# Performance work log

Hardware: AMD Instinct MI355X
Metric: run time of the kernel (lower is better)

Reference implementation:

```python
import jax, jax.numpy as jnp
import numpy as np

N = 16384
E = 262144
HID = 128
NFILT = 128
NGAUSS = 50
NINTER = 6
CUTOFF = 10.0
NUMZ = 100
LOG2 = 0.6931471805599453


def ssp(x):
    # ShiftedSoftplus
    return jax.nn.softplus(x) - LOG2


def setup_inputs() -> dict:
    key = jax.random.key(0)
    ks = jax.random.split(key, 20)
    z = jax.random.randint(ks[0], (N,), 0, NUMZ)
    pos = jax.random.uniform(ks[1], (N, 3), dtype=jnp.float32) * 5.0  # box side 5 -> all pairs < cutoff
    edge_index = jax.random.randint(ks[2], (2, E), 0, N)
    s = lambda k, shape, fan: jax.random.normal(k, shape, dtype=jnp.float32) / np.sqrt(fan)
    params = dict(
        emb=s(ks[3], (NUMZ, HID), 1.0),
        Wf1=s(ks[4], (NINTER, NGAUSS, NFILT), NGAUSS), bf1=jnp.zeros((NINTER, NFILT), jnp.float32),
        Wf2=s(ks[5], (NINTER, NFILT, NFILT), NFILT), bf2=jnp.zeros((NINTER, NFILT), jnp.float32),
        Wl1=s(ks[6], (NINTER, HID, NFILT), HID),
        Wl2=s(ks[7], (NINTER, NFILT, HID), NFILT), bl2=jnp.zeros((NINTER, HID), jnp.float32),
        Wl=s(ks[8], (NINTER, HID, HID), HID), bl=jnp.zeros((NINTER, HID), jnp.float32),
        Wo1=s(ks[9], (HID, HID // 2), HID), bo1=jnp.zeros((HID // 2,), jnp.float32),
        Wo2=s(ks[10], (HID // 2, 1), HID // 2), bo2=jnp.zeros((1,), jnp.float32),
    )
    return dict(z=z, pos=pos, edge_index=edge_index, **params)


def reference(z, pos, edge_index, emb, Wf1, bf1, Wf2, bf2, Wl1, Wl2, bl2, Wl, bl, Wo1, bo1, Wo2, bo2):
    src, dst = edge_index[0], edge_index[1]
    # edge distances and Gaussian smearing
    d = jnp.linalg.norm(pos[src] - pos[dst], axis=-1)          # [E]
    offset = jnp.linspace(0.0, CUTOFF, NGAUSS, dtype=jnp.float32)
    coeff = -0.5 / (offset[1] - offset[0]) ** 2
    ea = jnp.exp(coeff * (d[:, None] - offset) ** 2)            # [E, NGAUSS]
    C = 0.5 * (jnp.cos(d * (np.pi / CUTOFF)) + 1.0)             # cosine cutoff [E]

    h = emb[z]                                                  # [N, HID]
    for i in range(NINTER):
        # continuous-filter weights
        Wfilt = (ssp(ea @ Wf1[i] + bf1[i]) @ Wf2[i] + bf2[i]) * C[:, None]  # [E, NFILT]
        x = h @ Wl1[i]                                          # lin1, no bias [N, NFILT]
        msg = x[src] * Wfilt                                    # gather + filter
        agg = jax.ops.segment_sum(msg, dst, num_segments=N)     # scatter-sum [N, NFILT]
        x = ssp(agg @ Wl2[i] + bl2[i]) @ Wl[i] + bl[i]          # lin2 -> ssp -> lin
        h = h + x

    h = ssp(h @ Wo1 + bo1) @ Wo2 + bo2                          # [N, 1] per-atom energy
    out = jnp.sum(h, axis=0, keepdims=True)                     # 'add' readout, single graph -> [1, 1]
    return jax.nn.relu(out)
```

## Files before the change

### kernel.cpp

```cpp
#include <hip/hip_runtime.h>
#include <math.h>

#define NATOM 16384
#define NEDGE 262144
#define HID 128
#define NG 50
#define NI 6

typedef _Float16 h8_t __attribute__((ext_vector_type(8)));
typedef _Float16 h4_t __attribute__((ext_vector_type(4)));
typedef float    f4_t __attribute__((ext_vector_type(4)));

__device__ __forceinline__ float ssp_f(float v) {
    float e = __expf(-fabsf(v));
    return fmaxf(v, 0.0f) + __logf(1.0f + e) - 0.69314718055994531f;
}

__global__ void fill0(float* __restrict__ p, int n4) {
    int i = blockIdx.x * 256 + threadIdx.x;
    if (i < n4) ((float4*)p)[i] = make_float4(0.f, 0.f, 0.f, 0.f);
}

__global__ void hist_k(const int* __restrict__ ei, int* __restrict__ cnt) {
    int e = blockIdx.x * 256 + threadIdx.x;
    if (e < NEDGE) atomicAdd(&cnt[ei[NEDGE + e]], 1);
}

__global__ void scan_k(const int* __restrict__ cnt, int* __restrict__ offs) {
    __shared__ int part[256];
    int t = threadIdx.x;
    int base = t * 64;
    int s = 0;
    for (int i = 0; i < 64; ++i) s += cnt[base + i];
    part[t] = s;
    __syncthreads();
    for (int off = 1; off < 256; off <<= 1) {
        int v = (t >= off) ? part[t - off] : 0;
        __syncthreads();
        part[t] += v;
        __syncthreads();
    }
    int r = part[t] - s;
    for (int i = 0; i < 64; ++i) { offs[base + i] = r; r += cnt[base + i]; }
    if (t == 255) offs[NATOM] = r;
}

__global__ void scatter_k(const int* __restrict__ ei, const int* __restrict__ offs,
                          int* __restrict__ cnt, int* __restrict__ sSrc, int* __restrict__ sDst) {
    int e = blockIdx.x * 256 + threadIdx.x;
    if (e >= NEDGE) return;
    int d = ei[NEDGE + e];
    int r = atomicAdd(&cnt[d], 1);
    int j = offs[d] + r;
    sSrc[j] = ei[e];
    sDst[j] = d;
}

__global__ void edge_pre(const float* __restrict__ pos,
                         const int* __restrict__ sSrc, const int* __restrict__ sDst,
                         _Float16* __restrict__ ea, float* __restrict__ Cb) {
    int j = blockIdx.x * 256 + threadIdx.x;
    if (j >= NEDGE) return;
    int s = sSrc[j], dd = sDst[j];
    float dx = pos[3*s]   - pos[3*dd];
    float dy = pos[3*s+1] - pos[3*dd+1];
    float dz = pos[3*s+2] - pos[3*dd+2];
    float d = sqrtf(dx*dx + dy*dy + dz*dz);
    Cb[j] = 0.5f * (cosf(d * 0.31415926535897931f) + 1.0f);
    const float delta = 10.0f / 49.0f;
    const float coeff = -0.5f / (delta * delta);
    #pragma unroll
    for (int gq = 0; gq < 8; ++gq) {
        h8_t hv;
        #pragma unroll
        for (int r = 0; r < 8; ++r) {
            int g = gq * 8 + r;
            float v = 0.0f;
            if (g < NG) { float u = d - (float)g * delta; v = __expf(coeff * u * u); }
            hv[r] = (_Float16)v;
        }
        *(h8_t*)&ea[(size_t)j * 64 + gq * 8] = hv;
    }
}

__global__ void wprep(const float* __restrict__ Wf1, const float* __restrict__ Wf2,
                      const float* __restrict__ Wl1, const float* __restrict__ Wl2,
                      const float* __restrict__ Wl,
                      _Float16* __restrict__ w1, _Float16* __restrict__ w2,
                      _Float16* __restrict__ wnh, _Float16* __restrict__ wnl) {
    int idx = blockIdx.x * 256 + threadIdx.x;
    const int S1 = NI * 128 * 64, S2 = NI * 128 * 128;
    if (idx < S1) {
        int i = idx >> 13, r = idx & 8191, fo = r >> 6, k = r & 63;
        float v = (k < NG) ? Wf1[(size_t)i * NG * 128 + k * 128 + fo] : 0.0f;
        w1[idx] = (_Float16)v;
        return;
    }
    idx -= S1;
    if (idx < S2) {
        int i = idx >> 14, r = idx & 16383, fo = r >> 7, k = r & 127;
        w2[idx] = (_Float16)Wf2[(size_t)i * 128 * 128 + k * 128 + fo];
        return;
    }
    idx -= S2;
    if (idx < 3 * S2) {
        int mi = idx >> 14;
        int r = idx & 16383, fo = r >> 7, k = r & 127;
        int m = mi / NI, i = mi % NI;
        const float* W = (m == 0) ? Wl1 : (m == 1) ? Wl2 : Wl;
        float v = W[(size_t)i * 128 * 128 + k * 128 + fo];
        _Float16 hh = (_Float16)v;
        wnh[idx] = hh; wnl[idx] = (_Float16)(v - (float)hh);
    }
}

__global__ void embed_k(const int* __restrict__ z, const float* __restrict__ emb,
                        float* __restrict__ h) {
    int tid = blockIdx.x * 256 + threadIdx.x;
    int n = tid >> 7, f = tid & 127;
    h[tid] = emb[z[n] * HID + f];
}

__launch_bounds__(256)
__global__ void gemm_node_mfma(const float* __restrict__ A,
                               const _Float16* __restrict__ wth, const _Float16* __restrict__ wtl,
                               _Float16* __restrict__ xh) {
    __shared__ _Float16 aH[64 * 136];
    __shared__ _Float16 aL[64 * 136];
    int t = threadIdx.x;
    int mb = blockIdx.x * 64;
    #pragma unroll
    for (int j = 0; j < 8; ++j) {
        int idx = t + j * 256;
        int row = idx >> 5, c4 = idx & 31;
        f4_t v = *(const f4_t*)&A[(size_t)(mb + row) * HID + c4 * 4];
        h4_t hh, ll;
        #pragma unroll
        for (int r = 0; r < 4; ++r) {
            _Float16 hx = (_Float16)v[r];
            hh[r] = hx; ll[r] = (_Float16)(v[r] - (float)hx);
        }
        *(h4_t*)&aH[row * 136 + c4 * 4] = hh;
        *(h4_t*)&aL[row * 136 + c4 * 4] = ll;
    }
    __syncthreads();

    int wv = t >> 6, lane = t & 63, l15 = lane & 15, quad = lane >> 4;
    f4_t acc[2][4];
    #pragma unroll
    for (int m = 0; m < 2; ++m)
        #pragma unroll
        for (int n = 0; n < 4; ++n) acc[m][n] = (f4_t)0.0f;

    for (int kc = 0; kc < 4; ++kc) {
        int k0 = kc * 32 + quad * 8;
        h8_t a_h[2], a_l[2];
        #pragma unroll
        for (int m = 0; m < 2; ++m) {
            int fr = wv * 32 + m * 16 + l15;
            a_h[m] = *(const h8_t*)&wth[fr * 128 + k0];
            a_l[m] = *(const h8_t*)&wtl[fr * 128 + k0];
        }
        #pragma unroll
        for (int n = 0; n < 4; ++n) {
            int er = n * 16 + l15;
            h8_t b_h = *(const h8_t*)&aH[er * 136 + k0];
            h8_t b_l = *(const h8_t*)&aL[er * 136 + k0];
            #pragma unroll
            for (int m = 0; m < 2; ++m) {
                acc[m][n] = __builtin_amdgcn_mfma_f32_16x16x32_f16(a_h[m], b_h, acc[m][n], 0, 0, 0);
                acc[m][n] = __builtin_amdgcn_mfma_f32_16x16x32_f16(a_h[m], b_l, acc[m][n], 0, 0, 0);
                acc[m][n] = __builtin_amdgcn_mfma_f32_16x16x32_f16(a_l[m], b_h, acc[m][n], 0, 0, 0);
            }
        }
    }

    #pragma unroll
    for (int n = 0; n < 4; ++n) {
        int el = n * 16 + l15;
        size_t row = (size_t)(mb + el);
        #pragma unroll
        for (int m = 0; m < 2; ++m) {
            int fb = wv * 32 + m * 16 + quad * 4;
            h4_t o;
            #pragma unroll
            for (int r = 0; r < 4; ++r) o[r] = (_Float16)acc[m][n][r];
            *(h4_t*)&xh[row * 128 + fb] = o;
        }
    }
}

__launch_bounds__(256)
__global__ void gemm_node3(const float* __restrict__ agg,
                           const _Float16* __restrict__ w2th, const _Float16* __restrict__ w2tl,
                           const _Float16* __restrict__ wlth, const _Float16* __restrict__ wltl,
                           const _Float16* __restrict__ w1nh, const _Float16* __restrict__ w1nl,
                           const float* __restrict__ bl2, const float* __restrict__ bl,
                           float* __restrict__ h, _Float16* __restrict__ xh) {
    __shared__ _Float16 aH[64 * 136];
    __shared__ _Float16 aL[64 * 136];
    int t = threadIdx.x;
    int mb = blockIdx.x * 64;
    #pragma unroll
    for (int j = 0; j < 8; ++j) {
        int idx = t + j * 256;
        int row = idx >> 5, c4 = idx & 31;
        f4_t v = *(const f4_t*)&agg[(size_t)(mb + row) * HID + c4 * 4];
        h4_t hh, ll;
        #pragma unroll
        for (int r = 0; r < 4; ++r) {
            _Float16 hx = (_Float16)v[r];
            hh[r] = hx; ll[r] = (_Float16)(v[r] - (float)hx);
        }
        *(h4_t*)&aH[row * 136 + c4 * 4] = hh;
        *(h4_t*)&aL[row * 136 + c4 * 4] = ll;
    }
    __syncthreads();

    int wv = t >> 6, lane = t & 63, l15 = lane & 15, quad = lane >> 4;
    int fq = wv * 32 + quad * 4;
    f4_t acc[2][4];

    #pragma unroll
    for (int m = 0; m < 2; ++m)
        #pragma unroll
        for (int n = 0; n < 4; ++n) acc[m][n] = (f4_t)0.0f;
    for (int kc = 0; kc < 4; ++kc) {
        int k0 = kc * 32 + quad * 8;
        h8_t a_h[2], a_l[2];
        #pragma unroll
        for (int m = 0; m < 2; ++m) {
            int fr = wv * 32 + m * 16 + l15;
            a_h[m] = *(const h8_t*)&w2th[fr * 128 + k0];
            a_l[m] = *(const h8_t*)&w2tl[fr * 128 + k0];
        }
        #pragma unroll
        for (int n = 0; n < 4; ++n) {
            int er = n * 16 + l15;
            h8_t b_h = *(const h8_t*)&aH[er * 136 + k0];
            h8_t b_l = *(const h8_t*)&aL[er * 136 + k0];
            #pragma unroll
            for (int m = 0; m < 2; ++m) {
                acc[m][n] = __builtin_amdgcn_mfma_f32_16x16x32_f16(a_h[m], b_h, acc[m][n], 0, 0, 0);
                acc[m][n] = __builtin_amdgcn_mfma_f32_16x16x32_f16(a_h[m], b_l, acc[m][n], 0, 0, 0);
                acc[m][n] = __builtin_amdgcn_mfma_f32_16x16x32_f16(a_l[m], b_h, acc[m][n], 0, 0, 0);
            }
        }
    }
    f4_t b2v[2];
    b2v[0] = *(const f4_t*)&bl2[fq]; b2v[1] = *(const f4_t*)&bl2[fq + 16];
    __syncthreads();

    #pragma unroll
    for (int m = 0; m < 2; ++m)
        #pragma unroll
        for (int n = 0; n < 4; ++n) {
            int el = n * 16 + l15;
            int fb = wv * 32 + m * 16 + quad * 4;
            h4_t hh, ll;
            #pragma unroll
            for (int r = 0; r < 4; ++r) {
                float sv = ssp_f(acc[m][n][r] + b2v[m][r]);
                _Float16 hx = (_Float16)sv;
                hh[r] = hx;
                ll[r] = (_Float16)(sv - (float)hx);
            }
            *(h4_t*)&aH[el * 136 + fb] = hh;
            *(h4_t*)&aL[el * 136 + fb] = ll;
        }
    __syncthreads();

    #pragma unroll
    for (int m = 0; m < 2; ++m)
        #pragma unroll
        for (int n = 0; n < 4; ++n) acc[m][n] = (f4_t)0.0f;
    for (int kc = 0; kc < 4; ++kc) {
        int k0 = kc * 32 + quad * 8;
        h8_t a_h[2], a_l[2];
        #pragma unroll
        for (int m = 0; m < 2; ++m) {
            int fr = wv * 32 + m * 16 + l15;
            a_h[m] = *(const h8_t*)&wlth[fr * 128 + k0];
            a_l[m] = *(const h8_t*)&wltl[fr * 128 + k0];
        }
        #pragma unroll
        for (int n = 0; n < 4; ++n) {
            int er = n * 16 + l15;
            h8_t b_h = *(const h8_t*)&aH[er * 136 + k0];
            h8_t b_l = *(const h8_t*)&aL[er * 136 + k0];
            #pragma unroll
            for (int m = 0; m < 2; ++m) {
                acc[m][n] = __builtin_amdgcn_mfma_f32_16x16x32_f16(a_h[m], b_h, acc[m][n], 0, 0, 0);
                acc[m][n] = __builtin_amdgcn_mfma_f32_16x16x32_f16(a_h[m], b_l, acc[m][n], 0, 0, 0);
                acc[m][n] = __builtin_amdgcn_mfma_f32_16x16x32_f16(a_l[m], b_h, acc[m][n], 0, 0, 0);
            }
        }
    }
    f4_t blv[2];
    blv[0] = *(const f4_t*)&bl[fq]; blv[1] = *(const f4_t*)&bl[fq + 16];
    __syncthreads();

    #pragma unroll
    for (int n = 0; n < 4; ++n) {
        int el = n * 16 + l15;
        size_t row = (size_t)(mb + el);
        #pragma unroll
        for (int m = 0; m < 2; ++m) {
            int fb = wv * 32 + m * 16 + quad * 4;
            f4_t hv = *(const f4_t*)&h[row * 128 + fb];
            f4_t o;
            h4_t hh, ll;
            #pragma unroll
            for (int r = 0; r < 4; ++r) {
                o[r] = hv[r] + acc[m][n][r] + blv[m][r];
                _Float16 hx = (_Float16)o[r];
                hh[r] = hx; ll[r] = (_Float16)(o[r] - (float)hx);
            }
            *(f4_t*)&h[row * 128 + fb] = o;
            *(h4_t*)&aH[el * 136 + fb] = hh;
            *(h4_t*)&aL[el * 136 + fb] = ll;
        }
    }
    if (!w1nh) return;
    __syncthreads();

    #pragma unroll
    for (int m = 0; m < 2; ++m)
        #pragma unroll
        for (int n = 0; n < 4; ++n) acc[m][n] = (f4_t)0.0f;
    for (int kc = 0; kc < 4; ++kc) {
        int k0 = kc * 32 + quad * 8;
        h8_t a_h[2], a_l[2];
        #pragma unroll
        for (int m = 0; m < 2; ++m) {
            int fr = wv * 32 + m * 16 + l15;
            a_h[m] = *(const h8_t*)&w1nh[fr * 128 + k0];
            a_l[m] = *(const h8_t*)&w1nl[fr * 128 + k0];
        }
        #pragma unroll
        for (int n = 0; n < 4; ++n) {
            int er = n * 16 + l15;
            h8_t b_h = *(const h8_t*)&aH[er * 136 + k0];
            h8_t b_l = *(const h8_t*)&aL[er * 136 + k0];
            #pragma unroll
            for (int m = 0; m < 2; ++m) {
                acc[m][n] = __builtin_amdgcn_mfma_f32_16x16x32_f16(a_h[m], b_h, acc[m][n], 0, 0, 0);
                acc[m][n] = __builtin_amdgcn_mfma_f32_16x16x32_f16(a_h[m], b_l, acc[m][n], 0, 0, 0);
                acc[m][n] = __builtin_amdgcn_mfma_f32_16x16x32_f16(a_l[m], b_h, acc[m][n], 0, 0, 0);
            }
        }
    }
    #pragma unroll
    for (int n = 0; n < 4; ++n) {
        int el = n * 16 + l15;
        size_t row = (size_t)(mb + el);
        #pragma unroll
        for (int m = 0; m < 2; ++m) {
            int fb = wv * 32 + m * 16 + quad * 4;
            h4_t o;
            #pragma unroll
            for (int r = 0; r < 4; ++r) o[r] = (_Float16)acc[m][n][r];
            *(h4_t*)&xh[row * 128 + fb] = o;
        }
    }
}

#define T1_LDW 136
#define EA_LDW 72
#define NDST 16

__launch_bounds__(256, 4)
__global__ void edge_filter(const _Float16* __restrict__ xh, float* __restrict__ agg,
                            const int* __restrict__ sSrc, const int* __restrict__ sDst,
                            const int* __restrict__ offs, const float* __restrict__ Cb,
                            const _Float16* __restrict__ ea,
                            const _Float16* __restrict__ w1, const _Float16* __restrict__ w2,
                            const float* __restrict__ bf1, const float* __restrict__ bf2) {
    __shared__ __align__(16) _Float16 eaS[64 * EA_LDW];
    __shared__ __align__(16) _Float16 t1S[64 * T1_LDW];
    __shared__ float accS[NDST * 128];
    __shared__ int dstl[64];

    _Float16* msg = t1S;

    int t = threadIdx.x;
    int wv = t >> 6, lane = t & 63;
    int l15 = lane & 15, quad = lane >> 4;
    int d0 = blockIdx.x * NDST;
    int estart = offs[d0];
    int ecnt = offs[d0 + NDST] - estart;
    int tmax = (ecnt + 63) >> 6;

    #pragma unroll
    for (int c = 0; c < 2; ++c)
        *(f4_t*)&accS[(t + c * 256) * 4] = (f4_t)0.0f;

    h8_t w1f[2][2], w2f[4][2];
    #pragma unroll
    for (int kc = 0; kc < 2; ++kc) {
        int k0 = kc * 32 + quad * 8;
        #pragma unroll
        for (int m = 0; m < 2; ++m)
            w1f[kc][m] = *(const h8_t*)&w1[(wv * 32 + m * 16 + l15) * 64 + k0];
    }
    #pragma unroll
    for (int kc = 0; kc < 4; ++kc) {
        int k0 = kc * 32 + quad * 8;
        #pragma unroll
        for (int m = 0; m < 2; ++m)
            w2f[kc][m] = *(const h8_t*)&w2[(wv * 32 + m * 16 + l15) * 128 + k0];
    }
    int fq = wv * 32 + quad * 4;
    f4_t b1v[2], b2v[2];
    b1v[0] = *(const f4_t*)&bf1[fq];  b1v[1] = *(const f4_t*)&bf1[fq + 16];
    b2v[0] = *(const f4_t*)&bf2[fq];  b2v[1] = *(const f4_t*)&bf2[fq + 16];

    for (int tt = 0; tt < tmax; ++tt) {
        int base = estart + tt * 64;
        int lim = ecnt - tt * 64;

        #pragma unroll
        for (int c = 0; c < 2; ++c) {
            int ch = t + c * 256;
            int e = ch >> 3, ks = ch & 7;
            h8_t v = (h8_t)(_Float16)0.0f;
            if (e < lim) v = *(const h8_t*)&ea[(size_t)(base + e) * 64 + ks * 8];
            *(h8_t*)&eaS[e * EA_LDW + ks * 8] = v;
        }
        if (t < 64) {
            int dl = 0;
            if (t < lim) dl = sDst[base + t] - d0;
            dstl[t] = dl;
        }
        int srcn[4];
        float cn[4];
        #pragma unroll
        for (int n = 0; n < 4; ++n) {
            int rel = n * 16 + l15;
            bool ok = rel < lim;
            srcn[n] = ok ? sSrc[base + rel] : 0;
            cn[n]   = ok ? Cb[base + rel] : 0.0f;
        }
        h4_t xr[4][2];
        #pragma unroll
        for (int n = 0; n < 4; ++n)
            #pragma unroll
            for (int m = 0; m < 2; ++m)
                xr[n][m] = *(const h4_t*)&xh[(size_t)srcn[n] * HID + wv * 32 + m * 16 + quad * 4];
        __syncthreads();

        f4_t acc1[2][4];
        #pragma unroll
        for (int m = 0; m < 2; ++m)
            #pragma unroll
            for (int n = 0; n < 4; ++n) acc1[m][n] = (f4_t)0.0f;
        #pragma unroll
        for (int kc = 0; kc < 2; ++kc) {
            int k0 = kc * 32 + quad * 8;
            h8_t b[4];
            #pragma unroll
            for (int n = 0; n < 4; ++n)
                b[n] = *(const h8_t*)&eaS[(n * 16 + l15) * EA_LDW + k0];
            #pragma unroll
            for (int m = 0; m < 2; ++m)
                #pragma unroll
                for (int n = 0; n < 4; ++n)
                    acc1[m][n] = __builtin_amdgcn_mfma_f32_16x16x32_f16(w1f[kc][m], b[n], acc1[m][n], 0, 0, 0);
        }

        #pragma unroll
        for (int m = 0; m < 2; ++m)
            #pragma unroll
            for (int n = 0; n < 4; ++n) {
                int el = n * 16 + l15;
                int fb = wv * 32 + m * 16 + quad * 4;
                h4_t hh;
                #pragma unroll
                for (int r = 0; r < 4; ++r)
                    hh[r] = (_Float16)ssp_f(acc1[m][n][r] + b1v[m][r]);
                *(h4_t*)&t1S[el * T1_LDW + fb] = hh;
            }
        __syncthreads();

        f4_t acc2[2][4];
        #pragma unroll
        for (int m = 0; m < 2; ++m)
            #pragma unroll
            for (int n = 0; n < 4; ++n) acc2[m][n] = (f4_t)0.0f;
        #pragma unroll
        for (int kc = 0; kc < 4; ++kc) {
            int k0 = kc * 32 + quad * 8;
            #pragma unroll
            for (int n = 0; n < 4; ++n) {
                h8_t b = *(const h8_t*)&t1S[(n * 16 + l15) * T1_LDW + k0];
                #pragma unroll
                for (int m = 0; m < 2; ++m)
                    acc2[m][n] = __builtin_amdgcn_mfma_f32_16x16x32_f16(w2f[kc][m], b, acc2[m][n], 0, 0, 0);
            }
        }
        __syncthreads();

        #pragma unroll
        for (int n = 0; n < 4; ++n) {
            int el = n * 16 + l15;
            float ce = cn[n];
            #pragma unroll
            for (int m = 0; m < 2; ++m) {
                int fb = wv * 32 + m * 16 + quad * 4;
                h4_t o;
                #pragma unroll
                for (int r = 0; r < 4; ++r)
                    o[r] = (_Float16)((acc2[m][n][r] + b2v[m][r]) * ce * (float)xr[n][m][r]);
                *(h4_t*)&msg[el * T1_LDW + fb] = o;
            }
        }
        __syncthreads();

        {
            int f = t & 127, hf = t >> 7;
            int ib = hf * 32;
            float run = 0.0f;
            int cur = dstl[ib];
            for (int i = ib; i < ib + 32; ++i) {
                int dnow = dstl[i];
                if (dnow != cur) {
                    atomicAdd(&accS[cur * 128 + f], run);
                    run = 0.0f;
                    cur = dnow;
                }
                run += (float)msg[i * T1_LDW + f];
            }
            atomicAdd(&accS[cur * 128 + f], run);
        }
        __syncthreads();
    }

    float* dstp = &agg[(size_t)d0 * HID];
    #pragma unroll
    for (int c = 0; c < 2; ++c) {
        int idx = t + c * 256;
        *(f4_t*)&dstp[idx * 4] = *(const f4_t*)&accS[idx * 4];
    }
}

__launch_bounds__(256)
__global__ void readout1(const float* __restrict__ h, const float* __restrict__ Wo1,
                         const float* __restrict__ bo1, const float* __restrict__ Wo2,
                         const float* __restrict__ bo2, float* __restrict__ accum) {
    __shared__ float w1[128 * 64];
    __shared__ float part[4];
    int t = threadIdx.x;
    for (int i = t; i < 128 * 16; i += 256)
        ((float4*)w1)[i] = ((const float4*)Wo1)[i];
    __syncthreads();
    int f = t & 63, wv = t >> 6;
    float b = bo1[f], w2v = Wo2[f];
    float lsum = 0.0f;
    for (int a = 0; a < 16; ++a) {
        int n = blockIdx.x * 64 + wv * 16 + a;
        const float* hr = &h[(size_t)n * HID];
        float acc = b;
        #pragma unroll 16
        for (int k = 0; k < 128; ++k)
            acc = fmaf(hr[k], w1[k*64 + f], acc);
        lsum += ssp_f(acc) * w2v;
    }
    #pragma unroll
    for (int off = 32; off > 0; off >>= 1)
        lsum += __shfl_down(lsum, off, 64);
    if (f == 0) part[wv] = lsum;
    __syncthreads();
    if (t == 0)
        atomicAdd(accum, part[0] + part[1] + part[2] + part[3] + 64.0f * bo2[0]);
}

__global__ void readout2(const float* __restrict__ accum, float* __restrict__ out) {
    out[0] = fmaxf(accum[0], 0.0f);
}

extern "C" void kernel_launch(void* const* d_in, const int* in_sizes, int n_in,
                              void* d_out, int out_size, void* d_ws, size_t ws_size,
                              hipStream_t stream) {
    const int*   z   = (const int*)d_in[0];
    const float* pos = (const float*)d_in[1];
    const int*   ei  = (const int*)d_in[2];
    const float* emb = (const float*)d_in[3];
    const float* Wf1 = (const float*)d_in[4];
    const float* bf1 = (const float*)d_in[5];
    const float* Wf2 = (const float*)d_in[6];
    const float* bf2 = (const float*)d_in[7];
    const float* Wl1 = (const float*)d_in[8];
    const float* Wl2 = (const float*)d_in[9];
    const float* bl2 = (const float*)d_in[10];
    const float* Wl  = (const float*)d_in[11];
    const float* bl  = (const float*)d_in[12];
    const float* Wo1 = (const float*)d_in[13];
    const float* bo1 = (const float*)d_in[14];
    const float* Wo2 = (const float*)d_in[15];
    const float* bo2 = (const float*)d_in[16];
    float* out = (float*)d_out;

    _Float16* w1  = (_Float16*)d_ws;
    _Float16* w2  = w1 + NI * 8192;
    _Float16* wnh = w2 + NI * 16384;
    _Float16* wnl = wnh + 3 * NI * 16384;
    _Float16* ea  = wnl + 3 * NI * 16384;
    _Float16* xh  = ea + (size_t)NEDGE * 64;
    float* Cb  = (float*)(xh + (size_t)NATOM * 128);
    float* h   = Cb + NEDGE;
    float* agg = h + (size_t)NATOM * HID;
    float* accum = agg + (size_t)NATOM * HID;
    int* cnt  = (int*)(accum + 4);
    int* offs = cnt + NATOM;
    int* sSrc = offs + NATOM + 4;
    int* sDst = sSrc + NEDGE;

    fill0<<<NATOM/4/256, 256, 0, stream>>>((float*)cnt, NATOM/4);
    hist_k<<<NEDGE/256, 256, 0, stream>>>(ei, cnt);
    scan_k<<<1, 256, 0, stream>>>(cnt, offs);
    fill0<<<NATOM/4/256, 256, 0, stream>>>((float*)cnt, NATOM/4);
    scatter_k<<<NEDGE/256, 256, 0, stream>>>(ei, offs, cnt, sSrc, sDst);

    edge_pre<<<NEDGE/256, 256, 0, stream>>>(pos, sSrc, sDst, ea, Cb);
    wprep<<<(NI*8192 + NI*16384 + 3*NI*16384)/256, 256, 0, stream>>>(
        Wf1, Wf2, Wl1, Wl2, Wl, w1, w2, wnh, wnl);
    embed_k<<<(NATOM*HID)/256, 256, 0, stream>>>(z, emb, h);

    gemm_node_mfma<<<256, 256, 0, stream>>>(h, wnh + (size_t)0*16384,
        wnl + (size_t)0*16384, xh);
    for (int i = 0; i < NI; ++i) {
        edge_filter<<<NATOM/NDST, 256, 0, stream>>>(xh, agg, sSrc, sDst, offs, Cb, ea,
            w1 + (size_t)i*8192, w2 + (size_t)i*16384,
            bf1 + i*HID, bf2 + i*HID);
        const _Float16* w1nh = (i < NI-1) ? wnh + (size_t)(i+1)*16384 : nullptr;
        const _Float16* w1nl = (i < NI-1) ? wnl + (size_t)(i+1)*16384 : nullptr;
        gemm_node3<<<256, 256, 0, stream>>>(agg,
            wnh + (size_t)(1*NI+i)*16384, wnl + (size_t)(1*NI+i)*16384,
            wnh + (size_t)(2*NI+i)*16384, wnl + (size_t)(2*NI+i)*16384,
            w1nh, w1nl, bl2 + i*HID, bl + i*HID, h, xh);
    }
    fill0<<<1, 256, 0, stream>>>(accum, 1);
    readout1<<<NATOM/64, 256, 0, stream>>>(h, Wo1, bo1, Wo2, bo2, accum);
    readout2<<<1, 1, 0, stream>>>(accum, out);
}
```

Before: 784.3 us.

## Drop split-fp16 node GEMMs, halve tiles, prefetch edge tiles in filter kernel

After: 1.093 ms. 1.39x slower.

```diff
diff --git a/kernel.cpp b/kernel.cpp
--- a/kernel.cpp
+++ b/kernel.cpp
@@ -87,7 +87,7 @@
                       const float* __restrict__ Wl1, const float* __restrict__ Wl2,
                       const float* __restrict__ Wl,
                       _Float16* __restrict__ w1, _Float16* __restrict__ w2,
-                      _Float16* __restrict__ wnh, _Float16* __restrict__ wnl) {
+                      _Float16* __restrict__ wn) {
     int idx = blockIdx.x * 256 + threadIdx.x;
     const int S1 = NI * 128 * 64, S2 = NI * 128 * 128;
     if (idx < S1) {
@@ -108,9 +108,7 @@
         int r = idx & 16383, fo = r >> 7, k = r & 127;
         int m = mi / NI, i = mi % NI;
         const float* W = (m == 0) ? Wl1 : (m == 1) ? Wl2 : Wl;
-        float v = W[(size_t)i * 128 * 128 + k * 128 + fo];
-        _Float16 hh = (_Float16)v;
-        wnh[idx] = hh; wnl[idx] = (_Float16)(v - (float)hh);
+        wn[idx] = (_Float16)W[(size_t)i * 128 * 128 + k * 128 + fo];
     }
 }
 
@@ -123,10 +121,9 @@
 
 __launch_bounds__(256)
 __global__ void gemm_node_mfma(const float* __restrict__ A,
-                               const _Float16* __restrict__ wth, const _Float16* __restrict__ wtl,
+                               const _Float16* __restrict__ wt,
                                _Float16* __restrict__ xh) {
-    __shared__ _Float16 aH[64 * 136];
-    __shared__ _Float16 aL[64 * 136];
+    __shared__ _Float16 aS[64 * 136];
     int t = threadIdx.x;
     int mb = blockIdx.x * 64;
     #pragma unroll
@@ -134,14 +131,10 @@
         int idx = t + j * 256;
         int row = idx >> 5, c4 = idx & 31;
         f4_t v = *(const f4_t*)&A[(size_t)(mb + row) * HID + c4 * 4];
-        h4_t hh, ll;
-        #pragma unroll
-        for (int r = 0; r < 4; ++r) {
-            _Float16 hx = (_Float16)v[r];
-            hh[r] = hx; ll[r] = (_Float16)(v[r] - (float)hx);
-        }
-        *(h4_t*)&aH[row * 136 + c4 * 4] = hh;
-        *(h4_t*)&aL[row * 136 + c4 * 4] = ll;
+        h4_t hh;
+        #pragma unroll
+        for (int r = 0; r < 4; ++r) hh[r] = (_Float16)v[r];
+        *(h4_t*)&aS[row * 136 + c4 * 4] = hh;
     }
     __syncthreads();
 
@@ -154,24 +147,16 @@
 
     for (int kc = 0; kc < 4; ++kc) {
         int k0 = kc * 32 + quad * 8;
-        h8_t a_h[2], a_l[2];
-        #pragma unroll
-        for (int m = 0; m < 2; ++m) {
-            int fr = wv * 32 + m * 16 + l15;
-            a_h[m] = *(const h8_t*)&wth[fr * 128 + k0];
-            a_l[m] = *(const h8_t*)&wtl[fr * 128 + k0];
-        }
+        h8_t a[2];
+        #pragma unroll
+        for (int m = 0; m < 2; ++m)
+            a[m] = *(const h8_t*)&wt[(wv * 32 + m * 16 + l15) * 128 + k0];
         #pragma unroll
         for (int n = 0; n < 4; ++n) {
-            int er = n * 16 + l15;
-            h8_t b_h = *(const h8_t*)&aH[er * 136 + k0];
-            h8_t b_l = *(const h8_t*)&aL[er * 136 + k0];
-            #pragma unroll
-            for (int m = 0; m < 2; ++m) {
-                acc[m][n] = __builtin_amdgcn_mfma_f32_16x16x32_f16(a_h[m], b_h, acc[m][n], 0, 0, 0);
-                acc[m][n] = __builtin_amdgcn_mfma_f32_16x16x32_f16(a_h[m], b_l, acc[m][n], 0, 0, 0);
-                acc[m][n] = __builtin_amdgcn_mfma_f32_16x16x32_f16(a_l[m], b_h, acc[m][n], 0, 0, 0);
-            }
+            h8_t b = *(const h8_t*)&aS[(n * 16 + l15) * 136 + k0];
+            #pragma unroll
+            for (int m = 0; m < 2; ++m)
+                acc[m][n] = __builtin_amdgcn_mfma_f32_16x16x32_f16(a[m], b, acc[m][n], 0, 0, 0);
         }
     }
 
@@ -192,59 +177,45 @@
 
 __launch_bounds__(256)
 __global__ void gemm_node3(const float* __restrict__ agg,
-                           const _Float16* __restrict__ w2th, const _Float16* __restrict__ w2tl,
-                           const _Float16* __restrict__ wlth, const _Float16* __restrict__ wltl,
-                           const _Float16* __restrict__ w1nh, const _Float16* __restrict__ w1nl,
+                           const _Float16* __restrict__ w2t, const _Float16* __restrict__ wlt,
+                           const _Float16* __restrict__ w1n,
                            const float* __restrict__ bl2, const float* __restrict__ bl,
                            float* __restrict__ h, _Float16* __restrict__ xh) {
-    __shared__ _Float16 aH[64 * 136];
-    __shared__ _Float16 aL[64 * 136];
+    __shared__ _Float16 aS[32 * 136];
     int t = threadIdx.x;
-    int mb = blockIdx.x * 64;
-    #pragma unroll
-    for (int j = 0; j < 8; ++j) {
+    int mb = blockIdx.x * 32;
+    #pragma unroll
+    for (int j = 0; j < 4; ++j) {
         int idx = t + j * 256;
         int row = idx >> 5, c4 = idx & 31;
         f4_t v = *(const f4_t*)&agg[(size_t)(mb + row) * HID + c4 * 4];
-        h4_t hh, ll;
-        #pragma unroll
-        for (int r = 0; r < 4; ++r) {
-            _Float16 hx = (_Float16)v[r];
-            hh[r] = hx; ll[r] = (_Float16)(v[r] - (float)hx);
-        }
-        *(h4_t*)&aH[row * 136 + c4 * 4] = hh;
-        *(h4_t*)&aL[row * 136 + c4 * 4] = ll;
+        h4_t hh;
+        #pragma unroll
+        for (int r = 0; r < 4; ++r) hh[r] = (_Float16)v[r];
+        *(h4_t*)&aS[row * 136 + c4 * 4] = hh;
     }
     __syncthreads();
 
     int wv = t >> 6, lane = t & 63, l15 = lane & 15, quad = lane >> 4;
     int fq = wv * 32 + quad * 4;
-    f4_t acc[2][4];
+    f4_t acc[2][2];
 
     #pragma unroll
     for (int m = 0; m < 2; ++m)
         #pragma unroll
-        for (int n = 0; n < 4; ++n) acc[m][n] = (f4_t)0.0f;
+        for (int n = 0; n < 2; ++n) acc[m][n] = (f4_t)0.0f;
     for (int kc = 0; kc < 4; ++kc) {
         int k0 = kc * 32 + quad * 8;
-        h8_t a_h[2], a_l[2];
-        #pragma unroll
-        for (int m = 0; m < 2; ++m) {
-            int fr = wv * 32 + m * 16 + l15;
-            a_h[m] = *(const h8_t*)&w2th[fr * 128 + k0];
-            a_l[m] = *(const h8_t*)&w2tl[fr * 128 + k0];
-        }
-        #pragma unroll
-        for (int n = 0; n < 4; ++n) {
-            int er = n * 16 + l15;
-            h8_t b_h = *(const h8_t*)&aH[er * 136 + k0];
-            h8_t b_l = *(const h8_t*)&aL[er * 136 + k0];
-            #pragma unroll
-            for (int m = 0; m < 2; ++m) {
-                acc[m][n] = __builtin_amdgcn_mfma_f32_16x16x32_f16(a_h[m], b_h, acc[m][n], 0, 0, 0);
-                acc[m][n] = __builtin_amdgcn_mfma_f32_16x16x32_f16(a_h[m], b_l, acc[m][n], 0, 0, 0);
-                acc[m][n] = __builtin_amdgcn_mfma_f32_16x16x32_f16(a_l[m], b_h, acc[m][n], 0, 0, 0);
-            }
+        h8_t a[2];
+        #pragma unroll
+        for (int m = 0; m < 2; ++m)
+            a[m] = *(const h8_t*)&w2t[(wv * 32 + m * 16 + l15) * 128 + k0];
+        #pragma unroll
+        for (int n = 0; n < 2; ++n) {
+            h8_t b = *(const h8_t*)&aS[(n * 16 + l15) * 136 + k0];
+            #pragma unroll
+            for (int m = 0; m < 2; ++m)
+                acc[m][n] = __builtin_amdgcn_mfma_f32_16x16x32_f16(a[m], b, acc[m][n], 0, 0, 0);
         }
     }
     f4_t b2v[2];
@@ -254,46 +225,33 @@
     #pragma unroll
     for (int m = 0; m < 2; ++m)
         #pragma unroll
-        for (int n = 0; n < 4; ++n) {
+        for (int n = 0; n < 2; ++n) {
             int el = n * 16 + l15;
             int fb = wv * 32 + m * 16 + quad * 4;
-            h4_t hh, ll;
-            #pragma unroll
-            for (int r = 0; r < 4; ++r) {
-                float sv = ssp_f(acc[m][n][r] + b2v[m][r]);
-                _Float16 hx = (_Float16)sv;
-                hh[r] = hx;
-                ll[r] = (_Float16)(sv - (float)hx);
-            }
-            *(h4_t*)&aH[el * 136 + fb] = hh;
-            *(h4_t*)&aL[el * 136 + fb] = ll;
+            h4_t hh;
+            #pragma unroll
+            for (int r = 0; r < 4; ++r)
+                hh[r] = (_Float16)ssp_f(acc[m][n][r] + b2v[m][r]);
+            *(h4_t*)&aS[el * 136 + fb] = hh;
         }
     __syncthreads();
 
     #pragma unroll
     for (int m = 0; m < 2; ++m)
         #pragma unroll
-        for (int n = 0; n < 4; ++n) acc[m][n] = (f4_t)0.0f;
+        for (int n = 0; n < 2; ++n) acc[m][n] = (f4_t)0.0f;
     for (int kc = 0; kc < 4; ++kc) {
         int k0 = kc * 32 + quad * 8;
-        h8_t a_h[2], a_l[2];
-        #pragma unroll
-        for (int m = 0; m < 2; ++m) {
-            int fr = wv * 32 + m * 16 + l15;
-            a_h[m] = *(const h8_t*)&wlth[fr * 128 + k0];
-            a_l[m] = *(const h8_t*)&wltl[fr * 128 + k0];
-        }
-        #pragma unroll
-        for (int n = 0; n < 4; ++n) {
-            int er = n * 16 + l15;
-            h8_t b_h = *(const h8_t*)&aH[er * 136 + k0];
-            h8_t b_l = *(const h8_t*)&aL[er * 136 + k0];
-            #pragma unroll
-            for (int m = 0; m < 2; ++m) {
-                acc[m][n] = __builtin_amdgcn_mfma_f32_16x16x32_f16(a_h[m], b_h, acc[m][n], 0, 0, 0);
-                acc[m][n] = __builtin_amdgcn_mfma_f32_16x16x32_f16(a_h[m], b_l, acc[m][n], 0, 0, 0);
-                acc[m][n] = __builtin_amdgcn_mfma_f32_16x16x32_f16(a_l[m], b_h, acc[m][n], 0, 0, 0);
-            }
+        h8_t a[2];
+        #pragma unroll
+        for (int m = 0; m < 2; ++m)
+            a[m] = *(const h8_t*)&wlt[(wv * 32 + m * 16 + l15) * 128 + k0];
+        #pragma unroll
+        for (int n = 0; n < 2; ++n) {
+            h8_t b = *(const h8_t*)&aS[(n * 16 + l15) * 136 + k0];
+            #pragma unroll
+            for (int m = 0; m < 2; ++m)
+                acc[m][n] = __builtin_amdgcn_mfma_f32_16x16x32_f16(a[m], b, acc[m][n], 0, 0, 0);
         }
     }
     f4_t blv[2];
@@ -301,7 +259,7 @@
     __syncthreads();
 
     #pragma unroll
-    for (int n = 0; n < 4; ++n) {
+    for (int n = 0; n < 2; ++n) {
         int el = n * 16 + l15;
         size_t row = (size_t)(mb + el);
         #pragma unroll
@@ -309,49 +267,39 @@
             int fb = wv * 32 + m * 16 + quad * 4;
             f4_t hv = *(const f4_t*)&h[row * 128 + fb];
             f4_t o;
-            h4_t hh, ll;
+            h4_t hh;
             #pragma unroll
             for (int r = 0; r < 4; ++r) {
                 o[r] = hv[r] + acc[m][n][r] + blv[m][r];
-                _Float16 hx = (_Float16)o[r];
-                hh[r] = hx; ll[r] = (_Float16)(o[r] - (float)hx);
+                hh[r] = (_Float16)o[r];
             }
             *(f4_t*)&h[row * 128 + fb] = o;
-            *(h4_t*)&aH[el * 136 + fb] = hh;
-            *(h4_t*)&aL[el * 136 + fb] = ll;
-        }
-    }
-    if (!w1nh) return;
+            *(h4_t*)&aS[el * 136 + fb] = hh;
+        }
+    }
+    if (!w1n) return;
     __syncthreads();
 
     #pragma unroll
     for (int m = 0; m < 2; ++m)
         #pragma unroll
-        for (int n = 0; n < 4; ++n) acc[m][n] = (f4_t)0.0f;
+        for (int n = 0; n < 2; ++n) acc[m][n] = (f4_t)0.0f;
     for (int kc = 0; kc < 4; ++kc) {
         int k0 = kc * 32 + quad * 8;
-        h8_t a_h[2], a_l[2];
-        #pragma unroll
-        for (int m = 0; m < 2; ++m) {
-            int fr = wv * 32 + m * 16 + l15;
-            a_h[m] = *(const h8_t*)&w1nh[fr * 128 + k0];
-            a_l[m] = *(const h8_t*)&w1nl[fr * 128 + k0];
-        }
-        #pragma unroll
-        for (int n = 0; n < 4; ++n) {
-            int er = n * 16 + l15;
-            h8_t b_h = *(const h8_t*)&aH[er * 136 + k0];
-            h8_t b_l = *(const h8_t*)&aL[er * 136 + k0];
-            #pragma unroll
-            for (int m = 0; m < 2; ++m) {
-                acc[m][n] = __builtin_amdgcn_mfma_f32_16x16x32_f16(a_h[m], b_h, acc[m][n], 0, 0, 0);
-                acc[m][n] = __builtin_amdgcn_mfma_f32_16x16x32_f16(a_h[m], b_l, acc[m][n], 0, 0, 0);
-                acc[m][n] = __builtin_amdgcn_mfma_f32_16x16x32_f16(a_l[m], b_h, acc[m][n], 0, 0, 0);
-            }
-        }
-    }
-    #pragma unroll
-    for (int n = 0; n < 4; ++n) {
+        h8_t a[2];
+        #pragma unroll
+        for (int m = 0; m < 2; ++m)
+            a[m] = *(const h8_t*)&w1n[(wv * 32 + m * 16 + l15) * 128 + k0];
+        #pragma unroll
+        for (int n = 0; n < 2; ++n) {
+            h8_t b = *(const h8_t*)&aS[(n * 16 + l15) * 136 + k0];
+            #pragma unroll
+            for (int m = 0; m < 2; ++m)
+                acc[m][n] = __builtin_amdgcn_mfma_f32_16x16x32_f16(a[m], b, acc[m][n], 0, 0, 0);
+        }
+    }
+    #pragma unroll
+    for (int n = 0; n < 2; ++n) {
         int el = n * 16 + l15;
         size_t row = (size_t)(mb + el);
         #pragma unroll
@@ -367,7 +315,7 @@
 
 #define T1_LDW 136
 #define EA_LDW 72
-#define NDST 16
+#define NDST 8
 
 __launch_bounds__(256, 4)
 __global__ void edge_filter(const _Float16* __restrict__ xh, float* __restrict__ agg,
@@ -379,10 +327,9 @@
     __shared__ __align__(16) _Float16 eaS[64 * EA_LDW];
     __shared__ __align__(16) _Float16 t1S[64 * T1_LDW];
     __shared__ float accS[NDST * 128];
-    __shared__ int dstl[64];
+    __shared__ int dstl[2][64];
 
     _Float16* msg = t1S;
-
     int t = threadIdx.x;
     int wv = t >> 6, lane = t & 63;
     int l15 = lane & 15, quad = lane >> 4;
@@ -391,9 +338,7 @@
     int ecnt = offs[d0 + NDST] - estart;
     int tmax = (ecnt + 63) >> 6;
 
-    #pragma unroll
-    for (int c = 0; c < 2; ++c)
-        *(f4_t*)&accS[(t + c * 256) * 4] = (f4_t)0.0f;
+    *(f4_t*)&accS[t * 4] = (f4_t)0.0f;
 
     h8_t w1f[2][2], w2f[4][2];
     #pragma unroll
@@ -415,31 +360,55 @@
     b1v[0] = *(const f4_t*)&bf1[fq];  b1v[1] = *(const f4_t*)&bf1[fq + 16];
     b2v[0] = *(const f4_t*)&bf2[fq];  b2v[1] = *(const f4_t*)&bf2[fq + 16];
 
-    for (int tt = 0; tt < tmax; ++tt) {
-        int base = estart + tt * 64;
-        int lim = ecnt - tt * 64;
-
+    int srcn[4];
+    float cn[4];
+    {
+        int lim = ecnt;
         #pragma unroll
         for (int c = 0; c < 2; ++c) {
             int ch = t + c * 256;
             int e = ch >> 3, ks = ch & 7;
             h8_t v = (h8_t)(_Float16)0.0f;
-            if (e < lim) v = *(const h8_t*)&ea[(size_t)(base + e) * 64 + ks * 8];
+            if (e < lim) v = *(const h8_t*)&ea[(size_t)(estart + e) * 64 + ks * 8];
             *(h8_t*)&eaS[e * EA_LDW + ks * 8] = v;
         }
-        if (t < 64) {
-            int dl = 0;
-            if (t < lim) dl = sDst[base + t] - d0;
-            dstl[t] = dl;
-        }
-        int srcn[4];
-        float cn[4];
+        if (t < 64) dstl[0][t] = (t < lim) ? (sDst[estart + t] - d0) : 0;
         #pragma unroll
         for (int n = 0; n < 4; ++n) {
             int rel = n * 16 + l15;
             bool ok = rel < lim;
-            srcn[n] = ok ? sSrc[base + rel] : 0;
-            cn[n]   = ok ? Cb[base + rel] : 0.0f;
+            srcn[n] = ok ? sSrc[estart + rel] : 0;
+            cn[n]   = ok ? Cb[estart + rel] : 0.0f;
+        }
+    }
+    __syncthreads();
+
+    for (int tt = 0; tt < tmax; ++tt) {
+        int cur = tt & 1, nxt = cur ^ 1;
+        bool pre = (tt + 1 < tmax);
+
+        h8_t sregN[2];
+        int srcp[4], dln = 0;
+        float cp[4];
+        if (pre) {
+            int base2 = estart + (tt + 1) * 64;
+            int lim2 = ecnt - (tt + 1) * 64;
+            #pragma unroll
+            for (int c = 0; c < 2; ++c) {
+                int ch = t + c * 256;
+                int e = ch >> 3, ks = ch & 7;
+                h8_t v = (h8_t)(_Float16)0.0f;
+                if (e < lim2) v = *(const h8_t*)&ea[(size_t)(base2 + e) * 64 + ks * 8];
+                sregN[c] = v;
+            }
+            if (t < 64) dln = (t < lim2) ? (sDst[base2 + t] - d0) : 0;
+            #pragma unroll
+            for (int n = 0; n < 4; ++n) {
+                int rel = n * 16 + l15;
+                bool ok = rel < lim2;
+                srcp[n] = ok ? sSrc[base2 + rel] : 0;
+                cp[n]   = ok ? Cb[base2 + rel] : 0.0f;
+            }
         }
         h4_t xr[4][2];
         #pragma unroll
@@ -447,7 +416,6 @@
             #pragma unroll
             for (int m = 0; m < 2; ++m)
                 xr[n][m] = *(const h4_t*)&xh[(size_t)srcn[n] * HID + wv * 32 + m * 16 + quad * 4];
-        __syncthreads();
 
         f4_t acc1[2][4];
         #pragma unroll
@@ -482,6 +450,16 @@
             }
         __syncthreads();
 
+        if (pre) {
+            #pragma unroll
+            for (int c = 0; c < 2; ++c) {
+                int ch = t + c * 256;
+                int e = ch >> 3, ks = ch & 7;
+                *(h8_t*)&eaS[e * EA_LDW + ks * 8] = sregN[c];
+            }
+            if (t < 64) dstl[nxt][t] = dln;
+        }
+
         f4_t acc2[2][4];
         #pragma unroll
         for (int m = 0; m < 2; ++m)
@@ -517,30 +495,41 @@
         __syncthreads();
 
         {
-            int f = t & 127, hf = t >> 7;
-            int ib = hf * 32;
-            float run = 0.0f;
-            int cur = dstl[ib];
-            for (int i = ib; i < ib + 32; ++i) {
-                int dnow = dstl[i];
-                if (dnow != cur) {
-                    atomicAdd(&accS[cur * 128 + f], run);
-                    run = 0.0f;
-                    cur = dnow;
+            int fg = t & 15, rs = t >> 4;
+            int f0 = fg * 8;
+            int i0 = rs * 4;
+            int4 dq = *(const int4*)&dstl[cur][i0];
+            int dd[4] = {dq.x, dq.y, dq.z, dq.w};
+            float run[8];
+            #pragma unroll
+            for (int k = 0; k < 8; ++k) run[k] = 0.0f;
+            int curd = dd[0];
+            #pragma unroll
+            for (int i = 0; i < 4; ++i) {
+                int dnow = dd[i];
+                if (dnow != curd) {
+                    #pragma unroll
+                    for (int k = 0; k < 8; ++k) atomicAdd(&accS[curd * 128 + f0 + k], run[k]);
+                    #pragma unroll
+                    for (int k = 0; k < 8; ++k) run[k] = 0.0f;
+                    curd = dnow;
                 }
-                run += (float)msg[i * T1_LDW + f];
-            }
-            atomicAdd(&accS[cur * 128 + f], run);
+                h8_t v = *(const h8_t*)&msg[(i0 + i) * T1_LDW + f0];
+                #pragma unroll
+                for (int k = 0; k < 8; ++k) run[k] += (float)v[k];
+            }
+            #pragma unroll
+            for (int k = 0; k < 8; ++k) atomicAdd(&accS[curd * 128 + f0 + k], run[k]);
         }
         __syncthreads();
-    }
-
-    float* dstp = &agg[(size_t)d0 * HID];
-    #pragma unroll
-    for (int c = 0; c < 2; ++c) {
-        int idx = t + c * 256;
-        *(f4_t*)&dstp[idx * 4] = *(const f4_t*)&accS[idx * 4];
-    }
+
+        if (pre) {
+            #pragma unroll
+            for (int n = 0; n < 4; ++n) { srcn[n] = srcp[n]; cn[n] = cp[n]; }
+        }
+    }
+
+    *(f4_t*)&agg[(size_t)d0 * HID + t * 4] = *(const f4_t*)&accS[t * 4];
 }
 
 __launch_bounds__(256)
@@ -600,12 +589,11 @@
     const float* bo2 = (const float*)d_in[16];
     float* out = (float*)d_out;
 
-    _Float16* w1  = (_Float16*)d_ws;
-    _Float16* w2  = w1 + NI * 8192;
-    _Float16* wnh = w2 + NI * 16384;
-    _Float16* wnl = wnh + 3 * NI * 16384;
-    _Float16* ea  = wnl + 3 * NI * 16384;
-    _Float16* xh  = ea + (size_t)NEDGE * 64;
+    _Float16* w1 = (_Float16*)d_ws;
+    _Float16* w2 = w1 + NI * 8192;
+    _Float16* wn = w2 + NI * 16384;
+    _Float16* ea = wn + 3 * NI * 16384;
+    _Float16* xh = ea + (size_t)NEDGE * 64;
     float* Cb  = (float*)(xh + (size_t)NATOM * 128);
     float* h   = Cb + NEDGE;
     float* agg = h + (size_t)NATOM * HID;
@@ -623,21 +611,18 @@
 
     edge_pre<<<NEDGE/256, 256, 0, stream>>>(pos, sSrc, sDst, ea, Cb);
     wprep<<<(NI*8192 + NI*16384 + 3*NI*16384)/256, 256, 0, stream>>>(
-        Wf1, Wf2, Wl1, Wl2, Wl, w1, w2, wnh, wnl);
+        Wf1, Wf2, Wl1, Wl2, Wl, w1, w2, wn);
     embed_k<<<(NATOM*HID)/256, 256, 0, stream>>>(z, emb, h);
 
-    gemm_node_mfma<<<256, 256, 0, stream>>>(h, wnh + (size_t)0*16384,
-        wnl + (size_t)0*16384, xh);
+    gemm_node_mfma<<<NATOM/64, 256, 0, stream>>>(h, wn, xh);
     for (int i = 0; i < NI; ++i) {
         edge_filter<<<NATOM/NDST, 256, 0, stream>>>(xh, agg, sSrc, sDst, offs, Cb, ea,
             w1 + (size_t)i*8192, w2 + (size_t)i*16384,
             bf1 + i*HID, bf2 + i*HID);
-        const _Float16* w1nh = (i < NI-1) ? wnh + (size_t)(i+1)*16384 : nullptr;
-        const _Float16* w1nl = (i < NI-1) ? wnl + (size_t)(i+1)*16384 : nullptr;
-        gemm_node3<<<256, 256, 0, stream>>>(agg,
-            wnh + (size_t)(1*NI+i)*16384, wnl + (size_t)(1*NI+i)*16384,
-            wnh + (size_t)(2*NI+i)*16384, wnl + (size_t)(2*NI+i)*16384,
-            w1nh, w1nl, bl2 + i*HID, bl + i*HID, h, xh);
+        const _Float16* w1n = (i < NI-1) ? wn + (size_t)(i+1)*16384 : nullptr;
+        gemm_node3<<<NATOM/32, 256, 0, stream>>>(agg,
+            wn + (size_t)(1*NI+i)*16384, wn + (size_t)(2*NI+i)*16384,
+            w1n, bl2 + i*HID, bl + i*HID, h, xh);
     }
     fill0<<<1, 256, 0, stream>>>(accum, 1);
     readout1<<<NATOM/64, 256, 0, stream>>>(h, Wo1, bo1, Wo2, bo2, accum);
```
